# Kernel tuning notes

Measured on AMD Instinct MI355X. Metric: run time of the kernel, lower is better.

The kernel has to match this reference:

```python
import math
import jax, jax.numpy as jnp
import numpy as np


def setup_inputs() -> dict:
    key = jax.random.key(0)
    k1, k2, k3 = jax.random.split(key, 3)
    n, c, h, w = 4, 128, 64, 64
    return {
        "key": jax.random.normal(k1, (n, c, h, w), dtype=jnp.float32),
        "query": jax.random.normal(k2, (n, c, h, w), dtype=jnp.float32),
        "value": jax.random.normal(k3, (n, c, h, w), dtype=jnp.float32),
    }


def reference(key, query, value):
    n, c, h, w = key.shape
    c2 = value.shape[1]
    hw = h * w
    k = key.reshape(n, c, hw)      # (n, c, hw)
    q = query.reshape(n, c, hw)    # (n, c, hw)
    v = value.reshape(n, c2, hw)   # (n, c2, hw)
    # scores[n, s, t] = sum_c k[n,c,s] * q[n,c,t], scaled by sqrt(c)
    scores = jnp.einsum("ncs,nct->nst", k, q) / math.sqrt(c)
    # softmax over dim=-2 (the key-token axis s)
    p_attn = jax.nn.softmax(scores, axis=-2)
    # p_val[n, e, t] = sum_s v[n,e,s] * p_attn[n,s,t]
    p_val = jnp.einsum("nes,nst->net", v, p_attn)
    return p_val.reshape(n, c2, h, w)
```

## Files before the change

kernel.cpp:

```cpp
#include <hip/hip_runtime.h>


#define HW 4096
#define CC 128
#define KSCALE 0.12751743f
#define CEXP   8.656170245f
#define SMEMB  152576

typedef _Float16 half8  __attribute__((ext_vector_type(8)));
typedef _Float16 half4v __attribute__((ext_vector_type(4)));
typedef float    float4v __attribute__((ext_vector_type(4)));

__device__ __forceinline__ float fast_exp2(float x) {
  return __builtin_amdgcn_exp2f(x);
}

__device__ __forceinline__ void async_copy16(void* lds, const void* g) {
  __builtin_amdgcn_global_load_lds(
      (const __attribute__((address_space(1))) unsigned int*)g,
      (__attribute__((address_space(3))) unsigned int*)lds, 16, 0, 0);
}

__global__ __launch_bounds__(256)
void prepass(const float* __restrict__ K, const float* __restrict__ Q,
             const float* __restrict__ V, _Float16* __restrict__ KT,
             _Float16* __restrict__ QT, _Float16* __restrict__ Vh) {
  const int bid = blockIdx.x;
  const int tid = threadIdx.x;
  if (bid < 2048) {
    __shared__ float tile[32][65];
    const bool isK = bid < 1024;
    const int id = bid & 1023;
    const float* in = isK ? K : Q;
    _Float16* out = isK ? KT : QT;
    const float scale = isK ? KSCALE : 1.0f;
    const int c0 = (id & 3) << 5;
    const int s0 = ((id >> 2) & 63) << 6;
    const int b  = id >> 8;
    const float* ib = in + (size_t)b * CC * HW;
    _Float16* ob = out + (size_t)b * HW * CC;
    const int r  = tid >> 4;
    const int c4 = (tid & 15) * 4;
    *(float4*)&tile[r][c4]      = *(const float4*)(ib + (size_t)(c0 + r) * HW + s0 + c4);
    *(float4*)&tile[r + 16][c4] = *(const float4*)(ib + (size_t)(c0 + r + 16) * HW + s0 + c4);
    __syncthreads();
    const int s  = tid >> 2;
    const int c8 = (tid & 3) * 8;
    half8 h;
    #pragma unroll
    for (int k = 0; k < 8; ++k) h[k] = (_Float16)(tile[c8 + k][s] * scale);
    *(half8*)&ob[(size_t)(s0 + s) * CC + c0 + c8] = h;
  } else {
    const int id = bid - 2048;
    #pragma unroll
    for (int p = 0; p < 4; ++p) {
      const int f = id * 1024 + p * 256 + tid;
      const float4v v = *(const float4v*)(V + 4 * (size_t)f);
      half4v h;
      h.x = (_Float16)v.x; h.y = (_Float16)v.y; h.z = (_Float16)v.z; h.w = (_Float16)v.w;
      *(half4v*)(Vh + 4 * (size_t)f) = h;
    }
  }
}

__global__ __launch_bounds__(256, 4)
void attn_q4b(const _Float16* __restrict__ KT, const _Float16* __restrict__ QT,
              const _Float16* __restrict__ Vh, float* __restrict__ Opart,
              float* __restrict__ lpart) {
  __shared__ __align__(16) _Float16 sK[2][32][128];
  __shared__ __align__(16) _Float16 sV[2][128][32];
  __shared__ __align__(16) _Float16 sPT[2][2][16][40];
  __shared__ float sLred[2][2][32];

  const int bid = blockIdx.x;
  const int xcd = bid & 7;
  const int idx = bid >> 3;
  const int grp = xcd + 8 * (idx >> 6);
  const int q4  = grp >> 2;
  const int b   = grp & 3;
  const int tt0 = (idx & 63) << 6;
  const int soff = q4 << 10;
  const int tid  = threadIdx.x;
  const int w    = tid >> 6;
  const int lane = tid & 63;
  const int q    = lane >> 4;
  const int tc   = lane & 15;
  const int g2   = w >> 1;
  const int u    = w & 1;

  const _Float16* KTb = KT + (size_t)b * HW * CC;
  const _Float16* Vb  = Vh + (size_t)b * CC * HW;
  float* Op = Opart + (size_t)(q4 * 4 + b) * CC * HW;

  half8 qf2[2][4];
  {
    const _Float16* qb = QT + (size_t)b * HW * CC;
    #pragma unroll
    for (int f = 0; f < 2; ++f) {
      const _Float16* qp = qb + (size_t)(tt0 + 32 * g2 + 16 * f + tc) * CC + 8 * q;
      #pragma unroll
      for (int ks = 0; ks < 4; ++ks) qf2[f][ks] = *(const half8*)(qp + 32 * ks);
    }
  }

  const int krow_l = lane >> 4, kchn = lane & 15;
  const int vrow_l = lane >> 2, vchn = lane & 3;
  #define STAGE_S(sn, bufn)                                                     \
    {                                                                           \
      _Pragma("unroll")                                                         \
      for (int p = 0; p < 2; ++p) {                                             \
        const int kr = w * 8 + p * 4 + krow_l;                                  \
        const int kg = kchn ^ (kr & 15);                                        \
        async_copy16(&sK[bufn][w * 8 + p * 4][0],                               \
                     KTb + (size_t)(soff + (sn) + kr) * CC + kg * 8);           \
        const int vr = w * 32 + p * 16 + vrow_l;                                \
        const int vg = vchn ^ ((vr >> 1) & 3);                                  \
        async_copy16(&sV[bufn][w * 32 + p * 16][0],                             \
                     Vb + (size_t)vr * HW + soff + (sn) + vg * 8);              \
      }                                                                         \
    }

  STAGE_S(0, 0);

  float4v accO[4][2];
  #pragma unroll
  for (int i = 0; i < 4; ++i) {
    accO[i][0] = (float4v){0.f, 0.f, 0.f, 0.f};
    accO[i][1] = (float4v){0.f, 0.f, 0.f, 0.f};
  }
  float lf0 = 0.0f, lf1 = 0.0f;

  __syncthreads();

  for (int it = 0; it < 1024 / 32; ++it) {
    const int buf = it & 1;
    if (it + 1 < 1024 / 32) STAGE_S((it + 1) * 32, buf ^ 1);

    float4v acc0 = (float4v){0.f, 0.f, 0.f, 0.f};
    float4v acc1 = (float4v){0.f, 0.f, 0.f, 0.f};
    #pragma unroll
    for (int ks = 0; ks < 4; ++ks) {
      const half8 a = *(const half8*)&sK[buf][16 * u + tc][((4 * ks + q) ^ tc) * 8];
      acc0 = __builtin_amdgcn_mfma_f32_16x16x32_f16(a, qf2[0][ks], acc0, 0, 0, 0);
      acc1 = __builtin_amdgcn_mfma_f32_16x16x32_f16(a, qf2[1][ks], acc1, 0, 0, 0);
    }

    {
      const float p0 = fast_exp2(acc0.x - CEXP);
      const float p1 = fast_exp2(acc0.y - CEXP);
      const float p2 = fast_exp2(acc0.z - CEXP);
      const float p3 = fast_exp2(acc0.w - CEXP);
      lf0 += (p0 + p1) + (p2 + p3);
      half4v h;
      h.x = (_Float16)p0; h.y = (_Float16)p1; h.z = (_Float16)p2; h.w = (_Float16)p3;
      *(half4v*)&sPT[g2][0][tc][16 * u + 4 * q] = h;
    }
    {
      const float p0 = fast_exp2(acc1.x - CEXP);
      const float p1 = fast_exp2(acc1.y - CEXP);
      const float p2 = fast_exp2(acc1.z - CEXP);
      const float p3 = fast_exp2(acc1.w - CEXP);
      lf1 += (p0 + p1) + (p2 + p3);
      half4v h;
      h.x = (_Float16)p0; h.y = (_Float16)p1; h.z = (_Float16)p2; h.w = (_Float16)p3;
      *(half4v*)&sPT[g2][1][tc][16 * u + 4 * q] = h;
    }

    asm volatile("s_waitcnt lgkmcnt(0)\ns_barrier" ::: "memory");

    const half8 bp0 = *(const half8*)&sPT[g2][0][tc][8 * q];
    const half8 bp1 = *(const half8*)&sPT[g2][1][tc][8 * q];
    #pragma unroll
    for (int i = 0; i < 4; ++i) {
      const int e = 64 * u + 16 * i + tc;
      const half8 av = *(const half8*)&sV[buf][e][(q ^ ((e >> 1) & 3)) * 8];
      accO[i][0] = __builtin_amdgcn_mfma_f32_16x16x32_f16(av, bp0, accO[i][0], 0, 0, 0);
      accO[i][1] = __builtin_amdgcn_mfma_f32_16x16x32_f16(av, bp1, accO[i][1], 0, 0, 0);
    }

    __syncthreads();
  }

  lf0 += __shfl_xor(lf0, 16); lf0 += __shfl_xor(lf0, 32);
  lf1 += __shfl_xor(lf1, 16); lf1 += __shfl_xor(lf1, 32);
  if (lane < 16) {
    sLred[g2][u][tc]      = lf0;
    sLred[g2][u][16 + tc] = lf1;
  }
  __syncthreads();
  if (u == 0 && lane < 32)
    lpart[(size_t)(q4 * 4 + b) * HW + tt0 + 32 * g2 + lane] =
        sLred[g2][0][lane] + sLred[g2][1][lane];

  #pragma unroll
  for (int i = 0; i < 4; ++i)
    #pragma unroll
    for (int f = 0; f < 2; ++f) {
      const int e0 = 64 * u + 16 * i + 4 * q;
      const int t  = tt0 + 32 * g2 + 16 * f + tc;
      Op[(size_t)(e0 + 0) * HW + t] = accO[i][f].x;
      Op[(size_t)(e0 + 1) * HW + t] = accO[i][f].y;
      Op[(size_t)(e0 + 2) * HW + t] = accO[i][f].z;
      Op[(size_t)(e0 + 3) * HW + t] = accO[i][f].w;
    }
}

__global__ __launch_bounds__(256)
void merge4(const float* __restrict__ Op, const float* __restrict__ lp,
            float* __restrict__ out) {
  const int f   = blockIdx.x * 256 + threadIdx.x;
  const int row = f >> 10;
  const int t4  = (f & 1023) << 2;
  const int b   = row >> 7;
  float4v o = (float4v){0.f, 0.f, 0.f, 0.f};
  float4v l = (float4v){0.f, 0.f, 0.f, 0.f};
  #pragma unroll
  for (int k = 0; k < 4; ++k) {
    const float4v ok = *(const float4v*)(Op + ((size_t)k * 512 + row) * HW + t4);
    const float4v lk = *(const float4v*)(lp + ((size_t)k * 4 + b) * HW + t4);
    o.x += ok.x; o.y += ok.y; o.z += ok.z; o.w += ok.w;
    l.x += lk.x; l.y += lk.y; l.z += lk.z; l.w += lk.w;
  }
  float4v r;
  r.x = o.x / l.x; r.y = o.y / l.y; r.z = o.z / l.z; r.w = o.w / l.w;
  *(float4v*)(out + (size_t)row * HW + t4) = r;
}

__global__ __launch_bounds__(512, 4)
void attn_half(const _Float16* __restrict__ KT, const _Float16* __restrict__ QT,
               const _Float16* __restrict__ Vh, float* __restrict__ Opart,
               float* __restrict__ lpart) {
  __shared__ __align__(16) _Float16 sK[2][64][128];
  __shared__ __align__(16) _Float16 sV[2][128][64];
  __shared__ __align__(16) _Float16 sPT[4][16][72];
  __shared__ float sLred[2][4][32];

  const int bid  = blockIdx.x;
  const int xcd  = bid & 7;
  const int idx  = bid >> 3;
  const int half = xcd >> 2;
  const int b    = xcd & 3;
  const int tt0  = idx << 6;
  const int soff = half << 11;
  const int tid  = threadIdx.x;
  const int w    = tid >> 6;
  const int lane = tid & 63;
  const int q    = lane >> 4;
  const int tc   = lane & 15;
  const int g2   = w >> 2;
  const int sl   = (w >> 1) & 1;
  const int eh   = w & 1;
  const int j    = 2 * sl + eh;

  const _Float16* KTb = KT + (size_t)b * HW * CC;
  const _Float16* Vb  = Vh + (size_t)b * CC * HW;
  float* Op = Opart + (size_t)(half * 4 + b) * CC * HW;

  half8 qf2[2][4];
  {
    const _Float16* qb = QT + (size_t)b * HW * CC;
    #pragma unroll
    for (int f = 0; f < 2; ++f) {
      const _Float16* qp = qb + (size_t)(tt0 + 32 * g2 + 16 * f + tc) * CC + 8 * q;
      #pragma unroll
      for (int ks = 0; ks < 4; ++ks) qf2[f][ks] = *(const half8*)(qp + 32 * ks);
    }
  }

  const int krow_l = lane >> 4, kchn = lane & 15;
  const int vrow_l = lane >> 3, vchn = lane & 7;
  #define STAGE_H(sn, bufn)                                                     \
    {                                                                           \
      _Pragma("unroll")                                                         \
      for (int p = 0; p < 2; ++p) {                                             \
        const int kr = w * 8 + p * 4 + krow_l;                                  \
        const int kg = kchn ^ (kr & 15);                                        \
        async_copy16(&sK[bufn][w * 8 + p * 4][0],                               \
                     KTb + (size_t)(soff + (sn) + kr) * CC + kg * 8);           \
        const int vr = w * 16 + p * 8 + vrow_l;                                 \
        const int vg = vchn ^ (vr & 7);                                         \
        async_copy16(&sV[bufn][w * 16 + p * 8][0],                              \
                     Vb + (size_t)vr * HW + soff + (sn) + vg * 8);              \
      }                                                                         \
    }

  STAGE_H(0, 0);

  float4v accO[4][2];
  #pragma unroll
  for (int i = 0; i < 4; ++i) {
    accO[i][0] = (float4v){0.f, 0.f, 0.f, 0.f};
    accO[i][1] = (float4v){0.f, 0.f, 0.f, 0.f};
  }
  float lf0 = 0.0f, lf1 = 0.0f;

  __syncthreads();

  for (int it = 0; it < 2048 / 64; ++it) {
    const int buf = it & 1;
    if (it + 1 < 2048 / 64) STAGE_H((it + 1) * 64, buf ^ 1);

    float4v acc0 = (float4v){0.f, 0.f, 0.f, 0.f};
    float4v acc1 = (float4v){0.f, 0.f, 0.f, 0.f};
    #pragma unroll
    for (int ks = 0; ks < 4; ++ks) {
      const half8 a = *(const half8*)&sK[buf][16 * j + tc][((4 * ks + q) ^ tc) * 8];
      acc0 = __builtin_amdgcn_mfma_f32_16x16x32_f16(a, qf2[0][ks], acc0, 0, 0, 0);
      acc1 = __builtin_amdgcn_mfma_f32_16x16x32_f16(a, qf2[1][ks], acc1, 0, 0, 0);
    }

    {
      const float p0 = fast_exp2(acc0.x - CEXP);
      const float p1 = fast_exp2(acc0.y - CEXP);
      const float p2 = fast_exp2(acc0.z - CEXP);
      const float p3 = fast_exp2(acc0.w - CEXP);
      lf0 += (p0 + p1) + (p2 + p3);
      half4v h;
      h.x = (_Float16)p0; h.y = (_Float16)p1; h.z = (_Float16)p2; h.w = (_Float16)p3;
      *(half4v*)&sPT[2 * g2 + 0][tc][16 * j + 4 * q] = h;
    }
    {
      const float p0 = fast_exp2(acc1.x - CEXP);
      const float p1 = fast_exp2(acc1.y - CEXP);
      const float p2 = fast_exp2(acc1.z - CEXP);
      const float p3 = fast_exp2(acc1.w - CEXP);
      lf1 += (p0 + p1) + (p2 + p3);
      half4v h;
      h.x = (_Float16)p0; h.y = (_Float16)p1; h.z = (_Float16)p2; h.w = (_Float16)p3;
      *(half4v*)&sPT[2 * g2 + 1][tc][16 * j + 4 * q] = h;
    }

    asm volatile("s_waitcnt lgkmcnt(0)\ns_barrier" ::: "memory");

    const half8 bp0 = *(const half8*)&sPT[2 * g2 + 0][tc][32 * sl + 8 * q];
    const half8 bp1 = *(const half8*)&sPT[2 * g2 + 1][tc][32 * sl + 8 * q];
    #pragma unroll
    for (int i = 0; i < 4; ++i) {
      const int e = 64 * eh + 16 * i + tc;
      const half8 av = *(const half8*)&sV[buf][e][((4 * sl + q) ^ (tc & 7)) * 8];
      accO[i][0] = __builtin_amdgcn_mfma_f32_16x16x32_f16(av, bp0, accO[i][0], 0, 0, 0);
      accO[i][1] = __builtin_amdgcn_mfma_f32_16x16x32_f16(av, bp1, accO[i][1], 0, 0, 0);
    }

    __syncthreads();
  }

  lf0 += __shfl_xor(lf0, 16); lf0 += __shfl_xor(lf0, 32);
  lf1 += __shfl_xor(lf1, 16); lf1 += __shfl_xor(lf1, 32);
  const int widx = 2 * sl + eh;
  if (lane < 16) {
    sLred[g2][widx][tc]      = lf0;
    sLred[g2][widx][16 + tc] = lf1;
  }

  float* mbuf = (float*)&sK[0][0][0];
  const int slot = (2 * g2 + eh) * 2048;
  __syncthreads();
  if (sl == 1) {
    #pragma unroll
    for (int i = 0; i < 4; ++i)
      #pragma unroll
      for (int f = 0; f < 2; ++f) {
        const int col = (16 * f + tc) ^ (4 * q);
        const int rb  = slot + (16 * i + 4 * q) * 32;
        mbuf[rb + 0 * 32 + col] = accO[i][f].x;
        mbuf[rb + 1 * 32 + col] = accO[i][f].y;
        mbuf[rb + 2 * 32 + col] = accO[i][f].z;
        mbuf[rb + 3 * 32 + col] = accO[i][f].w;
      }
  }
  __syncthreads();
  if (sl == 0) {
    #pragma unroll
    for (int i = 0; i < 4; ++i)
      #pragma unroll
      for (int f = 0; f < 2; ++f) {
        const int col = (16 * f + tc) ^ (4 * q);
        const int rb  = slot + (16 * i + 4 * q) * 32;
        const int e0  = 64 * eh + 16 * i + 4 * q;
        const int t   = tt0 + 32 * g2 + 16 * f + tc;
        Op[(size_t)(e0 + 0) * HW + t] = accO[i][f].x + mbuf[rb + 0 * 32 + col];
        Op[(size_t)(e0 + 1) * HW + t] = accO[i][f].y + mbuf[rb + 1 * 32 + col];
        Op[(size_t)(e0 + 2) * HW + t] = accO[i][f].z + mbuf[rb + 2 * 32 + col];
        Op[(size_t)(e0 + 3) * HW + t] = accO[i][f].w + mbuf[rb + 3 * 32 + col];
      }
    if (eh == 0 && lane < 32) {
      lpart[(size_t)(half * 4 + b) * HW + tt0 + 32 * g2 + lane] =
          (sLred[g2][0][lane] + sLred[g2][1][lane]) +
          (sLred[g2][2][lane] + sLred[g2][3][lane]);
    }
  }
}

__global__ __launch_bounds__(256)
void merge_split(const float* __restrict__ Op, const float* __restrict__ lp,
                 float* __restrict__ out) {
  const int f   = blockIdx.x * 256 + threadIdx.x;
  const int row = f >> 10;
  const int t4  = (f & 1023) << 2;
  const int b   = row >> 7;
  const float4v oa = *(const float4v*)(Op + (size_t)row * HW + t4);
  const float4v ob = *(const float4v*)(Op + ((size_t)row + 512) * HW + t4);
  const float4v la = *(const float4v*)(lp + (size_t)b * HW + t4);
  const float4v lb = *(const float4v*)(lp + ((size_t)b + 4) * HW + t4);
  float4v o;
  o.x = (oa.x + ob.x) / (la.x + lb.x);
  o.y = (oa.y + ob.y) / (la.y + lb.y);
  o.z = (oa.z + ob.z) / (la.z + lb.z);
  o.w = (oa.w + ob.w) / (la.w + lb.w);
  *(float4v*)(out + (size_t)row * HW + t4) = o;
}

__device__ __forceinline__ _Float16* pK(char* s, int buf, int row) {
  return (_Float16*)s + ((size_t)buf * 128 + row) * 128;
}
__device__ __forceinline__ _Float16* pV(char* s, int buf, int row) {
  return (_Float16*)(s + 65536) + ((size_t)buf * 128 + row) * 128;
}
__device__ __forceinline__ _Float16* pP(char* s, int w, int t) {
  return (_Float16*)(s + 131072) + ((size_t)w * 16 + t) * 40;
}
__device__ __forceinline__ float* pL(char* s, int g, int sl) {
  return (float*)(s + 151552) + ((size_t)g * 4 + sl) * 16;
}

__global__ __launch_bounds__(1024, 4)
void attn_mfma(const _Float16* __restrict__ KT, const _Float16* __restrict__ QT,
               const _Float16* __restrict__ Vh, float* __restrict__ Og) {
  __shared__ __align__(16) char smem[SMEMB];
  const int bid = blockIdx.x, tid = threadIdx.x;
  const int b    = bid >> 6;
  const int tt0  = (bid & 63) << 6;
  const int w    = tid >> 6;
  const int lane = tid & 63;
  const int q    = lane >> 4;
  const int tc   = lane & 15;
  const int g    = w >> 2;
  const int sl   = w & 3;

  const _Float16* KTb = KT + (size_t)b * HW * CC;
  const _Float16* Vb  = Vh + (size_t)b * CC * HW;
  float* Ob = Og + (size_t)b * CC * HW;

  half8 qf[4];
  {
    const _Float16* qp = QT + (size_t)b * HW * CC + (size_t)(tt0 + 16 * g + tc) * CC + 8 * q;
    #pragma unroll
    for (int ks = 0; ks < 4; ++ks) qf[ks] = *(const half8*)(qp + 32 * ks);
  }

  const int r0    = w * 8;
  const int lrow  = lane >> 4;
  const int lchnk = lane & 15;
  auto STAGE = [&](int sn, int buf) {
    #pragma unroll
    for (int p = 0; p < 2; ++p) {
      const int row = r0 + p * 4 + lrow;
      const int gc  = lchnk ^ (row & 15);
      async_copy16(pK(smem, buf, r0 + p * 4), KTb + (size_t)(sn + row) * CC + gc * 8);
      async_copy16(pV(smem, buf, r0 + p * 4), Vb + (size_t)row * HW + sn + gc * 8);
    }
  };

  STAGE(0, 0);

  float4v accO[8];
  #pragma unroll
  for (int i2 = 0; i2 < 8; ++i2) accO[i2] = (float4v){0.f, 0.f, 0.f, 0.f};
  float l_part = 0.0f;

  __syncthreads();

  for (int it = 0; it < HW / 128; ++it) {
    const int buf = it & 1;
    if (it + 1 < HW / 128) STAGE((it + 1) * 128, buf ^ 1);

    float4v acc[2];
    acc[0] = (float4v){0.f, 0.f, 0.f, 0.f};
    acc[1] = (float4v){0.f, 0.f, 0.f, 0.f};
    #pragma unroll
    for (int ks = 0; ks < 4; ++ks) {
      #pragma unroll
      for (int jj = 0; jj < 2; ++jj) {
        const int row = 32 * sl + 16 * jj + tc;
        const half8 a = *(const half8*)(pK(smem, buf, row) + ((4 * ks + q) ^ tc) * 8);
        acc[jj] = __builtin_amdgcn_mfma_f32_16x16x32_f16(a, qf[ks], acc[jj], 0, 0, 0);
      }
    }

    #pragma unroll
    for (int jj = 0; jj < 2; ++jj) {
      const float p0 = fast_exp2(acc[jj].x - CEXP);
      const float p1 = fast_exp2(acc[jj].y - CEXP);
      const float p2 = fast_exp2(acc[jj].z - CEXP);
      const float p3 = fast_exp2(acc[jj].w - CEXP);
      l_part += (p0 + p1) + (p2 + p3);
      half4v h;
      h.x = (_Float16)p0; h.y = (_Float16)p1; h.z = (_Float16)p2; h.w = (_Float16)p3;
      *(half4v*)(pP(smem, w, tc) + 16 * jj + 4 * q) = h;
    }

    const half8 bp = *(const half8*)(pP(smem, w, tc) + 8 * q);
    #pragma unroll
    for (int i2 = 0; i2 < 8; ++i2) {
      const half8 av = *(const half8*)(pV(smem, buf, 16 * i2 + tc) + ((4 * sl + q) ^ tc) * 8);
      accO[i2] = __builtin_amdgcn_mfma_f32_16x16x32_f16(av, bp, accO[i2], 0, 0, 0);
    }

    __syncthreads();
  }

  l_part += __shfl_xor(l_part, 16);
  l_part += __shfl_xor(l_part, 32);
  if (lane < 16) pL(smem, g, sl)[tc] = l_part;

  float* mbuf = (float*)smem;
  if (sl != 0) {
    #pragma unroll
    for (int i2 = 0; i2 < 8; ++i2) {
      const int c4s = (4 * i2 + q) ^ ((tc & 7) << 2);
      *(float4v*)&mbuf[(size_t)(sl - 1) * 8192 + g * 2048 + tc * 128 + 4 * c4s] = accO[i2];
    }
  }
  __syncthreads();
  if (sl == 0) {
    const float li = 1.0f / (((pL(smem, g, 0)[tc] + pL(smem, g, 1)[tc]) +
                              (pL(smem, g, 2)[tc] + pL(smem, g, 3)[tc])));
    const int t = tt0 + 16 * g + tc;
    #pragma unroll
    for (int i2 = 0; i2 < 8; ++i2) {
      const int c4s = (4 * i2 + q) ^ ((tc & 7) << 2);
      float4v o = accO[i2];
      #pragma unroll
      for (int r = 0; r < 3; ++r) {
        const float4v m = *(const float4v*)&mbuf[(size_t)r * 8192 + g * 2048 + tc * 128 + 4 * c4s];
        o.x += m.x; o.y += m.y; o.z += m.z; o.w += m.w;
      }
      const int e0 = 16 * i2 + 4 * q;
      Ob[(size_t)(e0 + 0) * HW + t] = o.x * li;
      Ob[(size_t)(e0 + 1) * HW + t] = o.y * li;
      Ob[(size_t)(e0 + 2) * HW + t] = o.z * li;
      Ob[(size_t)(e0 + 3) * HW + t] = o.w * li;
    }
  }
}

extern "C" void kernel_launch(void* const* d_in, const int* in_sizes, int n_in,
                              void* d_out, int out_size, void* d_ws, size_t ws_size,
                              hipStream_t stream) {
  const float* key   = (const float*)d_in[0];
  const float* query = (const float*)d_in[1];
  const float* value = (const float*)d_in[2];
  float* out = (float*)d_out;

  const size_t TEN = (size_t)4 * HW * CC * sizeof(_Float16);
  const size_t OP4 = (size_t)4 * 4 * CC * HW * sizeof(float);
  const size_t LP4 = (size_t)4 * 4 * HW * sizeof(float);
  const size_t OP2 = (size_t)2 * 4 * CC * HW * sizeof(float);
  const size_t LP2 = (size_t)2 * 4 * HW * sizeof(float);
  _Float16* KT = (_Float16*)d_ws;
  _Float16* QT = (_Float16*)((char*)d_ws + TEN);
  _Float16* Vh = (_Float16*)((char*)d_ws + 2 * TEN);
  float* Opart = (float*)((char*)d_ws + 3 * TEN);

  prepass<<<dim3(2560), dim3(256), 0, stream>>>(key, query, value, KT, QT, Vh);
  if (ws_size >= 3 * TEN + OP4 + LP4) {
    float* lpart = (float*)((char*)d_ws + 3 * TEN + OP4);
    attn_q4b<<<dim3(1024), dim3(256), 0, stream>>>(KT, QT, Vh, Opart, lpart);
    merge4<<<dim3(2048), dim3(256), 0, stream>>>(Opart, lpart, out);
  } else if (ws_size >= 3 * TEN + OP2 + LP2) {
    float* lpart = (float*)((char*)d_ws + 3 * TEN + OP2);
    attn_half<<<dim3(512), dim3(512), 0, stream>>>(KT, QT, Vh, Opart, lpart);
    merge_split<<<dim3(2048), dim3(256), 0, stream>>>(Opart, lpart, out);
  } else {
    attn_mfma<<<dim3(256), dim3(1024), 0, stream>>>(KT, QT, Vh, out);
  }
}
```

Before: 128.1 us.

## Software-pipeline QK and PV stages with double-buffered P and one barrier per step

The attention loop is restructured so that each step issues the PV MMAs for the previous tile (from a double-buffered P buffer) before computing the scores for the current tile. This removes the mid-iteration barrier, leaving a single syncthreads per step, and splits the K and V async staging so V is loaded one step later. The prepass transpose now handles full 128-channel rows per block with fewer blocks, and occupancy is lowered to 3 blocks per CU to make room for the larger shared buffer and extra live registers. The restructuring adds LDS use and register pressure in exchange for better overlap of the matrix engine with the exp and LDS work.

```diff
diff --git a/kernel.cpp b/kernel.cpp
--- a/kernel.cpp
+++ b/kernel.cpp
@@ -27,31 +27,39 @@
              _Float16* __restrict__ QT, _Float16* __restrict__ Vh) {
   const int bid = blockIdx.x;
   const int tid = threadIdx.x;
-  if (bid < 2048) {
-    __shared__ float tile[32][65];
-    const bool isK = bid < 1024;
-    const int id = bid & 1023;
-    const float* in = isK ? K : Q;
-    _Float16* out = isK ? KT : QT;
+  if (bid < 1024) {
+    __shared__ float tile[32][130];
+    const bool isK = bid < 512;
+    const int id = bid & 511;
+    const int b  = id >> 7;
+    const int s0 = (id & 127) << 5;
+    const float* ib = (isK ? K : Q) + (size_t)b * CC * HW;
+    _Float16* ob = (isK ? KT : QT) + (size_t)b * HW * CC;
     const float scale = isK ? KSCALE : 1.0f;
-    const int c0 = (id & 3) << 5;
-    const int s0 = ((id >> 2) & 63) << 6;
-    const int b  = id >> 8;
-    const float* ib = in + (size_t)b * CC * HW;
-    _Float16* ob = out + (size_t)b * HW * CC;
-    const int r  = tid >> 4;
-    const int c4 = (tid & 15) * 4;
-    *(float4*)&tile[r][c4]      = *(const float4*)(ib + (size_t)(c0 + r) * HW + s0 + c4);
-    *(float4*)&tile[r + 16][c4] = *(const float4*)(ib + (size_t)(c0 + r + 16) * HW + s0 + c4);
+    #pragma unroll
+    for (int i = 0; i < 4; ++i) {
+      const int f  = i * 256 + tid;
+      const int c  = f >> 3;
+      const int sq = (f & 7) * 4;
+      const float4v v = *(const float4v*)(ib + (size_t)c * HW + s0 + sq);
+      tile[sq + 0][c] = v.x;
+      tile[sq + 1][c] = v.y;
+      tile[sq + 2][c] = v.z;
+      tile[sq + 3][c] = v.w;
+    }
     __syncthreads();
-    const int s  = tid >> 2;
-    const int c8 = (tid & 3) * 8;
-    half8 h;
-    #pragma unroll
-    for (int k = 0; k < 8; ++k) h[k] = (_Float16)(tile[c8 + k][s] * scale);
-    *(half8*)&ob[(size_t)(s0 + s) * CC + c0 + c8] = h;
+    #pragma unroll
+    for (int i = 0; i < 2; ++i) {
+      const int g  = i * 256 + tid;
+      const int s  = g >> 4;
+      const int c8 = (g & 15) * 8;
+      half8 h;
+      #pragma unroll
+      for (int k = 0; k < 8; ++k) h[k] = (_Float16)(tile[s][c8 + k] * scale);
+      *(half8*)&ob[(size_t)(s0 + s) * CC + c8] = h;
+    }
   } else {
-    const int id = bid - 2048;
+    const int id = bid - 1024;
     #pragma unroll
     for (int p = 0; p < 4; ++p) {
       const int f = id * 1024 + p * 256 + tid;
@@ -63,13 +71,13 @@
   }
 }
 
-__global__ __launch_bounds__(256, 4)
-void attn_q4b(const _Float16* __restrict__ KT, const _Float16* __restrict__ QT,
+__global__ __launch_bounds__(256, 3)
+void attn_q4p(const _Float16* __restrict__ KT, const _Float16* __restrict__ QT,
               const _Float16* __restrict__ Vh, float* __restrict__ Opart,
               float* __restrict__ lpart) {
   __shared__ __align__(16) _Float16 sK[2][32][128];
   __shared__ __align__(16) _Float16 sV[2][128][32];
-  __shared__ __align__(16) _Float16 sPT[2][2][16][40];
+  __shared__ __align__(16) _Float16 sPT[2][2][2][16][40];
   __shared__ float sLred[2][2][32];
 
   const int bid = blockIdx.x;
@@ -105,7 +113,7 @@
 
   const int krow_l = lane >> 4, kchn = lane & 15;
   const int vrow_l = lane >> 2, vchn = lane & 3;
-  #define STAGE_S(sn, bufn)                                                     \
+  #define STAGE_K(sn, bufn)                                                     \
     {                                                                           \
       _Pragma("unroll")                                                         \
       for (int p = 0; p < 2; ++p) {                                             \
@@ -113,6 +121,12 @@
         const int kg = kchn ^ (kr & 15);                                        \
         async_copy16(&sK[bufn][w * 8 + p * 4][0],                               \
                      KTb + (size_t)(soff + (sn) + kr) * CC + kg * 8);           \
+      }                                                                         \
+    }
+  #define STAGE_V(sn, bufn)                                                     \
+    {                                                                           \
+      _Pragma("unroll")                                                         \
+      for (int p = 0; p < 2; ++p) {                                             \
         const int vr = w * 32 + p * 16 + vrow_l;                                \
         const int vg = vchn ^ ((vr >> 1) & 3);                                  \
         async_copy16(&sV[bufn][w * 32 + p * 16][0],                             \
@@ -120,7 +134,7 @@
       }                                                                         \
     }
 
-  STAGE_S(0, 0);
+  STAGE_K(0, 0);
 
   float4v accO[4][2];
   #pragma unroll
@@ -132,53 +146,73 @@
 
   __syncthreads();
 
-  for (int it = 0; it < 1024 / 32; ++it) {
-    const int buf = it & 1;
-    if (it + 1 < 1024 / 32) STAGE_S((it + 1) * 32, buf ^ 1);
-
-    float4v acc0 = (float4v){0.f, 0.f, 0.f, 0.f};
-    float4v acc1 = (float4v){0.f, 0.f, 0.f, 0.f};
-    #pragma unroll
-    for (int ks = 0; ks < 4; ++ks) {
-      const half8 a = *(const half8*)&sK[buf][16 * u + tc][((4 * ks + q) ^ tc) * 8];
-      acc0 = __builtin_amdgcn_mfma_f32_16x16x32_f16(a, qf2[0][ks], acc0, 0, 0, 0);
-      acc1 = __builtin_amdgcn_mfma_f32_16x16x32_f16(a, qf2[1][ks], acc1, 0, 0, 0);
-    }
-
-    {
-      const float p0 = fast_exp2(acc0.x - CEXP);
-      const float p1 = fast_exp2(acc0.y - CEXP);
-      const float p2 = fast_exp2(acc0.z - CEXP);
-      const float p3 = fast_exp2(acc0.w - CEXP);
-      lf0 += (p0 + p1) + (p2 + p3);
-      half4v h;
-      h.x = (_Float16)p0; h.y = (_Float16)p1; h.z = (_Float16)p2; h.w = (_Float16)p3;
-      *(half4v*)&sPT[g2][0][tc][16 * u + 4 * q] = h;
-    }
-    {
-      const float p0 = fast_exp2(acc1.x - CEXP);
-      const float p1 = fast_exp2(acc1.y - CEXP);
-      const float p2 = fast_exp2(acc1.z - CEXP);
-      const float p3 = fast_exp2(acc1.w - CEXP);
-      lf1 += (p0 + p1) + (p2 + p3);
-      half4v h;
-      h.x = (_Float16)p0; h.y = (_Float16)p1; h.z = (_Float16)p2; h.w = (_Float16)p3;
-      *(half4v*)&sPT[g2][1][tc][16 * u + 4 * q] = h;
-    }
-
-    asm volatile("s_waitcnt lgkmcnt(0)\ns_barrier" ::: "memory");
-
-    const half8 bp0 = *(const half8*)&sPT[g2][0][tc][8 * q];
-    const half8 bp1 = *(const half8*)&sPT[g2][1][tc][8 * q];
+  #define PBODY(IT, PB)                                                         \
+  {                                                                             \
+    if ((IT) + 1 < 32) STAGE_K(((IT) + 1) * 32, (PB) ^ 1);                      \
+    STAGE_V((IT) * 32, PB);                                                     \
+    if ((IT) > 0) {                          \
+      const half8 bp0 = *(const half8*)&sPT[(PB) ^ 1][g2][0][tc][8 * q];        \
+      const half8 bp1 = *(const half8*)&sPT[(PB) ^ 1][g2][1][tc][8 * q];        \
+      _Pragma("unroll")                                                         \
+      for (int i = 0; i < 4; ++i) {                                             \
+        const int e = 64 * u + 16 * i + tc;                                     \
+        const half8 av = *(const half8*)&sV[(PB) ^ 1][e][(q ^ ((e >> 1) & 3)) * 8];\
+        accO[i][0] = __builtin_amdgcn_mfma_f32_16x16x32_f16(av, bp0, accO[i][0], 0, 0, 0);\
+        accO[i][1] = __builtin_amdgcn_mfma_f32_16x16x32_f16(av, bp1, accO[i][1], 0, 0, 0);\
+      }                                                                         \
+    }                                                                           \
+                                   \
+    float4v acc0 = (float4v){0.f, 0.f, 0.f, 0.f};                               \
+    float4v acc1 = (float4v){0.f, 0.f, 0.f, 0.f};                               \
+    _Pragma("unroll")                                                           \
+    for (int ks = 0; ks < 4; ++ks) {                                            \
+      const half8 a = *(const half8*)&sK[PB][16 * u + tc][((4 * ks + q) ^ tc) * 8];\
+      acc0 = __builtin_amdgcn_mfma_f32_16x16x32_f16(a, qf2[0][ks], acc0, 0, 0, 0);\
+      acc1 = __builtin_amdgcn_mfma_f32_16x16x32_f16(a, qf2[1][ks], acc1, 0, 0, 0);\
+    }                                                                           \
+    {                                                                           \
+      const float p0 = fast_exp2(acc0.x - CEXP);                                \
+      const float p1 = fast_exp2(acc0.y - CEXP);                                \
+      const float p2 = fast_exp2(acc0.z - CEXP);                                \
+      const float p3 = fast_exp2(acc0.w - CEXP);                                \
+      lf0 += (p0 + p1) + (p2 + p3);                                             \
+      half4v h;                                                                 \
+      h.x = (_Float16)p0; h.y = (_Float16)p1;                                   \
+      h.z = (_Float16)p2; h.w = (_Float16)p3;                                   \
+      *(half4v*)&sPT[PB][g2][0][tc][16 * u + 4 * q] = h;                        \
+    }                                                                           \
+    {                                                                           \
+      const float p0 = fast_exp2(acc1.x - CEXP);                                \
+      const float p1 = fast_exp2(acc1.y - CEXP);                                \
+      const float p2 = fast_exp2(acc1.z - CEXP);                                \
+      const float p3 = fast_exp2(acc1.w - CEXP);                                \
+      lf1 += (p0 + p1) + (p2 + p3);                                             \
+      half4v h;                                                                 \
+      h.x = (_Float16)p0; h.y = (_Float16)p1;                                   \
+      h.z = (_Float16)p2; h.w = (_Float16)p3;                                   \
+      *(half4v*)&sPT[PB][g2][1][tc][16 * u + 4 * q] = h;                        \
+    }                                                                           \
+    __syncthreads();            \
+  }
+
+  PBODY(0, 0)
+  for (int it2 = 1; it2 < 31; it2 += 2) {
+    PBODY(it2, 1)
+    PBODY(it2 + 1, 0)
+  }
+  PBODY(31, 1)
+  #undef PBODY
+
+  {
+    const half8 bp0 = *(const half8*)&sPT[1][g2][0][tc][8 * q];
+    const half8 bp1 = *(const half8*)&sPT[1][g2][1][tc][8 * q];
     #pragma unroll
     for (int i = 0; i < 4; ++i) {
       const int e = 64 * u + 16 * i + tc;
-      const half8 av = *(const half8*)&sV[buf][e][(q ^ ((e >> 1) & 3)) * 8];
+      const half8 av = *(const half8*)&sV[1][e][(q ^ ((e >> 1) & 3)) * 8];
       accO[i][0] = __builtin_amdgcn_mfma_f32_16x16x32_f16(av, bp0, accO[i][0], 0, 0, 0);
       accO[i][1] = __builtin_amdgcn_mfma_f32_16x16x32_f16(av, bp1, accO[i][1], 0, 0, 0);
     }
-
-    __syncthreads();
   }
 
   lf0 += __shfl_xor(lf0, 16); lf0 += __shfl_xor(lf0, 32);
@@ -563,10 +597,10 @@
   _Float16* Vh = (_Float16*)((char*)d_ws + 2 * TEN);
   float* Opart = (float*)((char*)d_ws + 3 * TEN);
 
-  prepass<<<dim3(2560), dim3(256), 0, stream>>>(key, query, value, KT, QT, Vh);
+  prepass<<<dim3(1536), dim3(256), 0, stream>>>(key, query, value, KT, QT, Vh);
   if (ws_size >= 3 * TEN + OP4 + LP4) {
     float* lpart = (float*)((char*)d_ws + 3 * TEN + OP4);
-    attn_q4b<<<dim3(1024), dim3(256), 0, stream>>>(KT, QT, Vh, Opart, lpart);
+    attn_q4p<<<dim3(1024), dim3(256), 0, stream>>>(KT, QT, Vh, Opart, lpart);
     merge4<<<dim3(2048), dim3(256), 0, stream>>>(Opart, lpart, out);
   } else if (ws_size >= 3 * TEN + OP2 + LP2) {
     float* lpart = (float*)((char*)d_ws + 3 * TEN + OP2);
```

Result: slower. 144.6 us (+12.9%).
